# Kernel tuning notes

Measured on AMD Instinct MI355X. Metric: run time of the kernel, lower is better.

Reference implementation:

```python
import jax, jax.numpy as jnp
import numpy as np

EPS = 1e-5      # F.layer_norm default eps
ALPHA = 0.08    # ALALLaDA blend coefficient


def setup_inputs() -> dict:
    key = jax.random.key(0)
    ks = jax.random.split(key, 6)
    B, S, D, K = 2, 2048, 2048, 8
    Fh = D // 4
    h_L = jax.random.normal(ks[0], (B, S, D), jnp.float32)
    # nonzero -> masked position (stands in for input_ids == 126336)
    mask = jax.random.randint(ks[1], (B, S), 0, 2).astype(jnp.int32)
    Wr = jax.random.normal(ks[2], (K, D), jnp.float32) / np.sqrt(D).astype(np.float32)
    br = jnp.zeros((K,), jnp.float32)
    W1 = jax.random.normal(ks[3], (K, D, Fh), jnp.float32) / np.sqrt(D).astype(np.float32)
    b1 = jnp.zeros((K, Fh), jnp.float32)
    W2 = jax.random.normal(ks[4], (K, Fh, D), jnp.float32) / np.sqrt(Fh).astype(np.float32)
    b2 = jnp.zeros((K, D), jnp.float32)
    return {"h_L": h_L, "mask": mask, "Wr": Wr, "br": br,
            "W1": W1, "b1": b1, "W2": W2, "b2": b2, "range_r": 8}


def _router_blend(h_L, Wr, br, W1, b1, W2, b2, mask, range_r):
    B, S, D = h_L.shape
    masked = mask != 0
    um = (~masked).astype(h_L.dtype)  # unmasked validity [B,S]
    # Per-token, per-expert outputs M[b,s,k,d]: Linear -> exact GELU -> Linear.
    pre = jnp.einsum('bsd,kdf->bskf', h_L, W1) + b1
    M = jnp.einsum('bskf,kfd->bskd', jax.nn.gelu(pre, approximate=False), W2) + b2
    # Routing weights at every position (softmax over K experts).
    w = jax.nn.softmax(jnp.einsum('bsd,kd->bsk', h_L, Wr) + br, axis=-1)
    # Accumulate weighted expert outputs over the +/-range_r neighbor window,
    # counting only unmasked neighbors. Fixed small loop over 2r offsets.
    num = jnp.zeros((B, S, D), h_L.dtype)
    cnt = jnp.zeros((B, S), h_L.dtype)
    for o in range(-range_r, range_r + 1):
        if o == 0:
            continue
        if o > 0:  # neighbor t = a + o: shift left, zero-pad tail
            Mo = jnp.pad(M[:, o:], ((0, 0), (0, o), (0, 0), (0, 0)))
            vo = jnp.pad(um[:, o:], ((0, 0), (0, o)))
        else:      # neighbor t = a + o (o<0): shift right, zero-pad head
            Mo = jnp.pad(M[:, :o], ((0, 0), (-o, 0), (0, 0), (0, 0)))
            vo = jnp.pad(um[:, :o], ((0, 0), (-o, 0)))
        num = num + vo[..., None] * jnp.einsum('bsk,bskd->bsd', w, Mo)
        cnt = cnt + vo
    has = cnt > 0
    mean = num / jnp.maximum(cnt, 1.0)[..., None]   # mean over valid neighbors
    # layer_norm over d_model, no affine
    mu = mean.mean(-1, keepdims=True)
    var = jnp.mean((mean - mu) ** 2, axis=-1, keepdims=True)
    ln = (mean - mu) / jnp.sqrt(var + EPS)
    # delta is written only at masked positions that had >=1 neighbor
    delta = jnp.where((masked & has)[..., None], ln, 0.0)
    return h_L + ALPHA * delta


def reference(h_L, mask, Wr, br, W1, b1, W2, b2, range_r):
    return _router_blend(h_L, Wr, br, W1, b1, W2, b2, mask, range_r)
```

## Files before the change

kernel.cpp:

```cpp
#include <hip/hip_runtime.h>
#include <hip/hip_bf16.h>
#include <math.h>


#define ALPHA 0.08f
#define EPS 1e-5f

typedef __attribute__((ext_vector_type(8))) __bf16 bf16x8;
typedef __attribute__((ext_vector_type(8))) short short8;
typedef __attribute__((ext_vector_type(4))) float f32x4;

__device__ __forceinline__ unsigned short f2bf(float f) {
  unsigned u = __float_as_uint(f);
  u += 0x7fffu + ((u >> 16) & 1u);
  return (unsigned short)(u >> 16);
}
__device__ __forceinline__ float bf2f(unsigned short b) {
  return __uint_as_float(((unsigned)b) << 16);
}

#define GLD16(gptr, lptr)                                                     \
  __builtin_amdgcn_global_load_lds(                                           \
      (const __attribute__((address_space(1))) void*)(gptr),                  \
      (__attribute__((address_space(3))) void*)(lptr), 16, 0, 0)

#define LD8(p) __builtin_bit_cast(bf16x8, *(const short8*)(p))

__device__ __forceinline__ int wave_incl_scan(int v, int lane) {
#pragma unroll
  for (int off = 1; off < 64; off <<= 1) {
    int t = __shfl_up(v, off);
    if (lane >= off) v += t;
  }
  return v;
}

__global__ __launch_bounds__(256) void prep_kernel(
    const float* __restrict__ h, const int* __restrict__ mask,
    const float* __restrict__ Wr, const float* __restrict__ br,
    const float* __restrict__ W1, const float* __restrict__ W2,
    const int* __restrict__ rptr, float* __restrict__ w,
    unsigned short* __restrict__ hbc, unsigned short* __restrict__ B1t,
    unsigned short* __restrict__ B2t, int* __restrict__ ru,
    int* __restrict__ msk_idx, int* __restrict__ pos2row,
    int* __restrict__ counts) {
  const int bid = blockIdx.x;
  const int tid = threadIdx.x;
  const int lane = tid & 63, wv = tid >> 6;

  if (bid < 16384) {
    __shared__ float tile[32][33];
    int id = bid;
    const float* src;
    unsigned short* dst;
    int C, c0, r0;
    size_t dstStride;
    if (id < 8192) {
      const int k = id >> 10, rem = id & 1023;
      src = W1 + (size_t)k * 2048 * 512;
      dst = B1t + (size_t)k * 512 * 2048;
      C = 512; dstStride = 2048;
      c0 = (rem >> 6) * 32; r0 = (rem & 63) * 32;
    } else {
      id -= 8192;
      const int k = id >> 10, rem = id & 1023;
      src = W2 + (size_t)k * 512 * 2048;
      dst = B2t + (size_t)k * 512;
      C = 2048; dstStride = 4096;
      c0 = (rem >> 4) * 32; r0 = (rem & 15) * 32;
    }
    const int tx = tid & 31, ty = tid >> 5;
#pragma unroll
    for (int i = 0; i < 4; ++i)
      tile[ty + 8 * i][tx] = src[(size_t)(r0 + ty + 8 * i) * C + (c0 + tx)];
    __syncthreads();
#pragma unroll
    for (int i = 0; i < 4; ++i) {
      const int c = c0 + ty + 8 * i;
      dst[(size_t)c * dstStride + (size_t)(r0 + tx)] =
          f2bf(tile[tx][ty + 8 * i]);
    }
    return;
  }

  if (bid < 20480) {
    const int a = bid - 16384;
    const size_t base = (size_t)a * 2048;
    const int d0 = tid * 8;
    float hv[8];
    *(float4*)(hv) = *(const float4*)(h + base + d0);
    *(float4*)(hv + 4) = *(const float4*)(h + base + d0 + 4);
    float acc[8];
#pragma unroll
    for (int k = 0; k < 8; ++k) {
      float wvv[8];
      *(float4*)(wvv) = *(const float4*)(Wr + (size_t)k * 2048 + d0);
      *(float4*)(wvv + 4) = *(const float4*)(Wr + (size_t)k * 2048 + d0 + 4);
      float s = 0.f;
#pragma unroll
      for (int j = 0; j < 8; ++j) s += hv[j] * wvv[j];
      acc[k] = s;
    }
    int c0n = 0;
    {
      const int4* m4p = (const int4*)mask;
#pragma unroll
      for (int q = 0; q < 4; ++q) {
        const int4 v = m4p[tid * 4 + q];
        const int b0 = tid * 16 + q * 4;
        c0n += (v.x == 0 && b0 + 0 < a);
        c0n += (v.y == 0 && b0 + 1 < a);
        c0n += (v.z == 0 && b0 + 2 < a);
        c0n += (v.w == 0 && b0 + 3 < a);
      }
    }
#pragma unroll
    for (int off = 32; off > 0; off >>= 1) {
      c0n += __shfl_down(c0n, off);
#pragma unroll
      for (int k = 0; k < 8; ++k) acc[k] += __shfl_down(acc[k], off);
    }
    __shared__ float red[4][8];
    __shared__ float logits[8];
    __shared__ int rucnt[4];
    __shared__ int rubc;
    if (lane == 0) {
#pragma unroll
      for (int k = 0; k < 8; ++k) red[wv][k] = acc[k];
      rucnt[wv] = c0n;
    }
    __syncthreads();
    if (tid < 8)
      logits[tid] =
          red[0][tid] + red[1][tid] + red[2][tid] + red[3][tid] + br[tid];
    if (tid == 0) rubc = rucnt[0] + rucnt[1] + rucnt[2] + rucnt[3];
    __syncthreads();
    if (tid == 0) {
      float mx = logits[0];
#pragma unroll
      for (int k = 1; k < 8; ++k) mx = fmaxf(mx, logits[k]);
      float e[8], se = 0.f;
#pragma unroll
      for (int k = 0; k < 8; ++k) {
        e[k] = expf(logits[k] - mx);
        se += e[k];
      }
      const float is = 1.f / se;
#pragma unroll
      for (int k = 0; k < 8; ++k) w[(size_t)a * 8 + k] = e[k] * is;
    }
    if (mask[a] == 0) {
      const int i = rubc;
      short8 o;
#pragma unroll
      for (int j = 0; j < 8; ++j) o[j] = (short)f2bf(hv[j]);
      *(short8*)(hbc + (size_t)i * 2048 + d0) = o;
    }
    return;
  }

  {
    __shared__ int sru[4097];
    __shared__ int wsum[4];
    __shared__ int wsum2[4];
    const int t0 = tid * 16;
    int mv[16];
    {
      const int4* p = (const int4*)mask;
#pragma unroll
      for (int q = 0; q < 4; ++q) {
        const int4 v = p[tid * 4 + q];
        mv[q * 4 + 0] = v.x; mv[q * 4 + 1] = v.y;
        mv[q * 4 + 2] = v.z; mv[q * 4 + 3] = v.w;
      }
    }
    int f[16];
    int c = 0;
#pragma unroll
    for (int e = 0; e < 16; ++e) { f[e] = (mv[e] == 0); c += f[e]; }
    const int isc = wave_incl_scan(c, lane);
    if (lane == 63) wsum[wv] = isc;
    __syncthreads();
    if (tid == 0) {
      int accs = 0;
#pragma unroll
      for (int i = 0; i < 4; ++i) { int v = wsum[i]; wsum[i] = accs; accs += v; }
      sru[4096] = accs;
      ru[4096] = accs;
      counts[0] = accs;
    }
    __syncthreads();
    int ex = wsum[wv] + isc - c;
#pragma unroll
    for (int e = 0; e < 16; ++e) {
      sru[t0 + e] = ex;
      ru[t0 + e] = ex;
      ex += f[e];
    }
    __syncthreads();
    const int r = rptr[0];
    int g[16];
    int c2 = 0;
#pragma unroll
    for (int e = 0; e < 16; ++e) {
      const int t = t0 + e;
      const int s = t & 2047, tb = t & ~2047;
      const int lo = max(s - r, 0), hi = min(s + r, 2047);
      const int cnt = sru[tb + hi + 1] - sru[tb + lo];
      g[e] = (mv[e] != 0 && cnt > 0) ? 1 : 0;
      c2 += g[e];
    }
    const int isc2 = wave_incl_scan(c2, lane);
    if (lane == 63) wsum2[wv] = isc2;
    __syncthreads();
    if (tid == 0) {
      int accs = 0;
#pragma unroll
      for (int i = 0; i < 4; ++i) { int v = wsum2[i]; wsum2[i] = accs; accs += v; }
      counts[1] = accs;
    }
    __syncthreads();
    int ex2 = wsum2[wv] + isc2 - c2;
#pragma unroll
    for (int e = 0; e < 16; ++e) {
      const int t = t0 + e;
      pos2row[t] = g[e] ? ex2 : -1;
      if (g[e]) msk_idx[ex2] = t;
      ex2 += g[e];
    }
  }
}

template <int EPI>
__global__ __launch_bounds__(256, 4) void gemm_bt_kernel(
    const unsigned short* __restrict__ A, const unsigned short* __restrict__ Bt,
    float* __restrict__ Cf0, float* __restrict__ Cf1,
    unsigned short* __restrict__ Cb, const float* __restrict__ bias,
    const int* __restrict__ counts, int cidx, int N, int Kstride, int Kd) {
  const int Mlim = counts[cidx];
  const int bm = blockIdx.y * 64;
  if (bm >= Mlim) return;
  const int bn = blockIdx.x * 128;
  const int kofs = blockIdx.z * Kd;
  constexpr int SBUF = 6144;
  __shared__ __align__(16) unsigned short L[3 * SBUF];
  const int tid = threadIdx.x;
  const int lane = tid & 63;
  const int wid = tid >> 6;
  const int wr = wid >> 1;
  const int wc = wid & 1;

  f32x4 acc[2][4];
#pragma unroll
  for (int m = 0; m < 2; ++m)
#pragma unroll
    for (int n = 0; n < 4; ++n) acc[m][n] = (f32x4){0.f, 0.f, 0.f, 0.f};

  const int l4 = lane >> 2;
  const int scol = (lane & 3) * 8;
  const unsigned short* gA0 =
      A + (size_t)(bm + wid * 16 + l4) * Kstride + kofs + scol;
  const unsigned short* gB0 =
      Bt + (size_t)(bn + wid * 32 + l4) * Kstride + kofs + scol;
  const unsigned short* gB1 = gB0 + (size_t)16 * Kstride;

  const int koff = (lane >> 4) * 8;
  const int aoff = (wr * 32 + (lane & 15)) * 32 + koff;
  const int boff = 2048 + (wc * 64 + (lane & 15)) * 32 + koff;

#define STAGE(buf, t)                                                         \
  {                                                                           \
    const int k0_ = (t) << 5;                                                 \
    unsigned short* la_ = L + (buf) * SBUF + wid * 512;                       \
    unsigned short* lb_ = L + (buf) * SBUF + 2048 + wid * 1024;               \
    GLD16(gA0 + k0_, la_);                                                    \
    GLD16(gB0 + k0_, lb_);                                                    \
    GLD16(gB1 + k0_, lb_ + 512);                                              \
  }

#define COMPUTE(buf)                                                          \
  {                                                                           \
    const unsigned short* bb_ = L + (buf) * SBUF;                             \
    bf16x8 af[2], bfr[4];                                                     \
    _Pragma("unroll") for (int m = 0; m < 2; ++m) af[m] =                     \
        LD8(bb_ + aoff + m * 512);                                            \
    _Pragma("unroll") for (int n = 0; n < 4; ++n) bfr[n] =                    \
        LD8(bb_ + boff + n * 512);                                            \
    _Pragma("unroll") for (int m = 0; m < 2; ++m)                             \
        _Pragma("unroll") for (int n = 0; n < 4; ++n) acc[m][n] =             \
            __builtin_amdgcn_mfma_f32_16x16x32_bf16(af[m], bfr[n],            \
                                                    acc[m][n], 0, 0, 0);      \
  }

  const int nt = Kd >> 5;
  STAGE(0, 0);
  STAGE(1, 1);
  int cb = 0, sb = 2;
#pragma unroll 1
  for (int t = 0; t < nt - 2; ++t) {
    asm volatile("s_waitcnt vmcnt(3)" ::: "memory");
    __builtin_amdgcn_s_barrier();
    __builtin_amdgcn_sched_barrier(0);
    STAGE(sb, t + 2);
    COMPUTE(cb);
    cb = (cb == 2) ? 0 : cb + 1;
    sb = (sb == 2) ? 0 : sb + 1;
  }
  asm volatile("s_waitcnt vmcnt(3)" ::: "memory");
  __builtin_amdgcn_s_barrier();
  __builtin_amdgcn_sched_barrier(0);
  COMPUTE(cb);
  cb = (cb == 2) ? 0 : cb + 1;
  asm volatile("s_waitcnt vmcnt(0)" ::: "memory");
  __builtin_amdgcn_s_barrier();
  __builtin_amdgcn_sched_barrier(0);
  COMPUTE(cb);
#undef STAGE
#undef COMPUTE

  float* __restrict__ Cf = (blockIdx.z == 0) ? Cf0 : Cf1;
  const int r0 = bm + wr * 32 + (lane >> 4) * 4;
  const int c0 = bn + wc * 64 + (lane & 15);
#pragma unroll
  for (int m = 0; m < 2; ++m) {
#pragma unroll
    for (int n = 0; n < 4; ++n) {
      const int col = c0 + n * 16;
#pragma unroll
      for (int ii = 0; ii < 4; ++ii) {
        const int row = r0 + m * 16 + ii;
        if (row >= Mlim) continue;
        const size_t off = (size_t)row * N + col;
        float v = acc[m][n][ii];
        if (EPI == 1) {
          v += bias[col];
          v = 0.5f * v * (1.0f + erff(v * 0.70710678118654752f));
          Cb[off] = f2bf(v);
        } else {
          Cf[off] = v;
        }
      }
    }
  }
}

__global__ __launch_bounds__(256) void window_kernel(
    const unsigned short* __restrict__ Act_c, const float* __restrict__ w,
    const int* __restrict__ ru, const int* __restrict__ pos2row,
    const int* __restrict__ rptr, unsigned short* __restrict__ G_c) {
  const int tid = threadIdx.x;
  const int b = blockIdx.y >> 7;
  const int seg = blockIdx.y & 127;
  const int s0 = seg * 16;
  const int tb = b * 2048;
  const int cbase = blockIdx.x * 2048 + tid * 8;
  const int kx = cbase >> 9;
  const int r = rptr[0];

  float W[8] = {0.f, 0.f, 0.f, 0.f, 0.f, 0.f, 0.f, 0.f};
  for (int t = s0 - r; t <= s0 + r; ++t) {
    if (t < 0 || t > 2047) continue;
    const int j = ru[tb + t];
    if (ru[tb + t + 1] > j) {
      const short8 v = *(const short8*)(Act_c + (size_t)j * 4096 + cbase);
#pragma unroll
      for (int e = 0; e < 8; ++e) W[e] += bf2f((unsigned short)v[e]);
    }
  }
#pragma unroll 1
  for (int i = 0; i < 16; ++i) {
    const int t = s0 + i;
    const int a = tb + t;
    const int rowo = pos2row[a];
    if (rowo >= 0) {
      const float wv = w[(size_t)a * 8 + kx];
      short8 o8;
#pragma unroll
      for (int e = 0; e < 8; ++e) o8[e] = (short)f2bf(W[e] * wv);
      *(short8*)(G_c + (size_t)rowo * 4096 + cbase) = o8;
    }
    const int tin = t + r + 1;
    if (tin < 2048) {
      const int j = ru[tb + tin];
      if (ru[tb + tin + 1] > j) {
        const short8 v = *(const short8*)(Act_c + (size_t)j * 4096 + cbase);
#pragma unroll
        for (int e = 0; e < 8; ++e) W[e] += bf2f((unsigned short)v[e]);
      }
    }
    const int tout = t - r;
    if (tout >= 0) {
      const int j = ru[tb + tout];
      if (ru[tb + tout + 1] > j) {
        const short8 v = *(const short8*)(Act_c + (size_t)j * 4096 + cbase);
#pragma unroll
        for (int e = 0; e < 8; ++e) W[e] -= bf2f((unsigned short)v[e]);
      }
    }
  }
}

__global__ void final_kernel(const float* __restrict__ h,
                             const int* __restrict__ pos2row,
                             const float* __restrict__ w,
                             const float* __restrict__ b2,
                             const float* __restrict__ p0,
                             const float* __restrict__ p1,
                             const int* __restrict__ ru,
                             const int* __restrict__ rptr,
                             float* __restrict__ out) {
  const int a = blockIdx.x;
  const int tid = threadIdx.x;
  const int lane = tid & 63, wid = tid >> 6;
  const size_t base = (size_t)a * 2048;
  const int d0 = tid * 8;
  const int row = pos2row[a];
  if (row < 0) {
    const float4 x0 = *(const float4*)(h + base + d0);
    const float4 x1 = *(const float4*)(h + base + d0 + 4);
    *(float4*)(out + base + d0) = x0;
    *(float4*)(out + base + d0 + 4) = x1;
    return;
  }
  const int s = a & 2047;
  const int tb = a & ~2047;
  const int r = rptr[0];
  const int lo = max(s - r, 0), hi = min(s + r, 2047);
  const int cnt = ru[tb + hi + 1] - ru[tb + lo];
  float wk[8];
#pragma unroll
  for (int k = 0; k < 8; ++k) wk[k] = w[(size_t)a * 8 + k];
  const float cntf = (float)cnt;
  const float icnt = 1.0f / cntf;
  float mval[8];
  float s1 = 0.f, s2 = 0.f;
#pragma unroll
  for (int j = 0; j < 8; ++j) {
    const int d = d0 + j;
    float wb2 = 0.f;
#pragma unroll
    for (int k = 0; k < 8; ++k) wb2 += wk[k] * b2[(size_t)k * 2048 + d];
    const size_t po = (size_t)row * 2048 + d;
    const float v = (p0[po] + p1[po] + cntf * wb2) * icnt;
    mval[j] = v;
    s1 += v;
    s2 += v * v;
  }
#pragma unroll
  for (int off = 32; off > 0; off >>= 1) {
    s1 += __shfl_down(s1, off);
    s2 += __shfl_down(s2, off);
  }
  __shared__ float red[8];
  if (lane == 0) {
    red[wid] = s1;
    red[4 + wid] = s2;
  }
  __syncthreads();
  const float S1 = red[0] + red[1] + red[2] + red[3];
  const float S2 = red[4] + red[5] + red[6] + red[7];
  const float mu = S1 * (1.0f / 2048.0f);
  const float var = S2 * (1.0f / 2048.0f) - mu * mu;
  const float rin = rsqrtf(var + EPS);
#pragma unroll
  for (int j = 0; j < 8; ++j) {
    const int d = d0 + j;
    out[base + d] = h[base + d] + ALPHA * ((mval[j] - mu) * rin);
  }
}

extern "C" void kernel_launch(void* const* d_in, const int* in_sizes, int n_in,
                              void* d_out, int out_size, void* d_ws,
                              size_t ws_size, hipStream_t stream) {
  const float* h = (const float*)d_in[0];
  const int* mask = (const int*)d_in[1];
  const float* Wr = (const float*)d_in[2];
  const float* br = (const float*)d_in[3];
  const float* W1 = (const float*)d_in[4];
  const float* b1 = (const float*)d_in[5];
  const float* W2 = (const float*)d_in[6];
  const float* b2 = (const float*)d_in[7];
  const int* rptr = (const int*)d_in[8];
  float* out = (float*)d_out;

  char* ws = (char*)d_ws;
  unsigned short* hbc = (unsigned short*)(ws + 0);
  unsigned short* B1t = (unsigned short*)(ws + 16777216);
  unsigned short* B2t = (unsigned short*)(ws + 33554432);
  unsigned short* Act_c = (unsigned short*)(ws + 50331648);
  unsigned short* G_c = (unsigned short*)(ws + 83886080);
  float* p0 = (float*)(ws + 50331648);
  float* p1 = (float*)(ws + 0);
  float* wbuf = (float*)(ws + 117440512);
  int* ru = (int*)(ws + 117571584);
  int* msk_idx = ru + 4100;
  int* pos2row = msk_idx + 4096;
  int* counts = pos2row + 4096;

  prep_kernel<<<20481, 256, 0, stream>>>(h, mask, Wr, br, W1, W2, rptr, wbuf,
                                         hbc, B1t, B2t, ru, msk_idx, pos2row,
                                         counts);
  gemm_bt_kernel<1><<<dim3(32, 64, 1), 256, 0, stream>>>(
      hbc, B1t, nullptr, nullptr, Act_c, b1, counts, 0, 4096, 2048, 2048);
  window_kernel<<<dim3(2, 256), 256, 0, stream>>>(Act_c, wbuf, ru, pos2row,
                                                  rptr, G_c);
  gemm_bt_kernel<0><<<dim3(16, 64, 2), 256, 0, stream>>>(
      G_c, B2t, p0, p1, nullptr, nullptr, counts, 1, 2048, 4096, 2048);
  final_kernel<<<4096, 256, 0, stream>>>(h, pos2row, wbuf, b2, p0, p1, ru,
                                         rptr, out);
}
```

Baseline: 338.5 us.

## Enlarge GEMM tiles to 128x256 with 8 waves and phased ping-pong schedule

```diff
diff --git a/kernel.cpp b/kernel.cpp
--- a/kernel.cpp
+++ b/kernel.cpp
@@ -232,97 +232,149 @@
 }
 
 template <int EPI>
-__global__ __launch_bounds__(256, 4) void gemm_bt_kernel(
+__global__ __launch_bounds__(512, 2) void gemm8p_kernel(
     const unsigned short* __restrict__ A, const unsigned short* __restrict__ Bt,
     float* __restrict__ Cf0, float* __restrict__ Cf1,
     unsigned short* __restrict__ Cb, const float* __restrict__ bias,
     const int* __restrict__ counts, int cidx, int N, int Kstride, int Kd) {
   const int Mlim = counts[cidx];
-  const int bm = blockIdx.y * 64;
+  const int bm = blockIdx.y * 128;
   if (bm >= Mlim) return;
-  const int bn = blockIdx.x * 128;
+  const int bn = blockIdx.x * 256;
   const int kofs = blockIdx.z * Kd;
-  constexpr int SBUF = 6144;
+  constexpr int SA = 8192;
+  constexpr int SBUF = 24576;
   __shared__ __align__(16) unsigned short L[3 * SBUF];
   const int tid = threadIdx.x;
   const int lane = tid & 63;
   const int wid = tid >> 6;
-  const int wr = wid >> 1;
-  const int wc = wid & 1;
-
-  f32x4 acc[2][4];
-#pragma unroll
-  for (int m = 0; m < 2; ++m)
+  const int wr = wid >> 2;
+  const int wc = wid & 3;
+
+  f32x4 acc[4][4];
+#pragma unroll
+  for (int m = 0; m < 4; ++m)
 #pragma unroll
     for (int n = 0; n < 4; ++n) acc[m][n] = (f32x4){0.f, 0.f, 0.f, 0.f};
 
-  const int l4 = lane >> 2;
-  const int scol = (lane & 3) * 8;
-  const unsigned short* gA0 =
-      A + (size_t)(bm + wid * 16 + l4) * Kstride + kofs + scol;
-  const unsigned short* gB0 =
-      Bt + (size_t)(bn + wid * 32 + l4) * Kstride + kofs + scol;
-  const unsigned short* gB1 = gB0 + (size_t)16 * Kstride;
-
-  const int koff = (lane >> 4) * 8;
-  const int aoff = (wr * 32 + (lane & 15)) * 32 + koff;
-  const int boff = 2048 + (wc * 64 + (lane & 15)) * 32 + koff;
-
-#define STAGE(buf, t)                                                         \
+  const int trow = tid >> 3;
+  const int scol = ((tid & 7) ^ (trow & 7)) * 8;
+  const unsigned short* gA =
+      A + (size_t)(bm + trow) * Kstride + kofs + scol;
+  const unsigned short* gB =
+      Bt + (size_t)(bn + trow) * Kstride + kofs + scol;
+  unsigned short* const ld0 = (unsigned short*)L + tid * 8;
+
+  const int x7 = lane & 7;
+  const int t16 = lane >> 4;
+  const int s0 = (t16 ^ x7) * 8;
+  const int s1 = ((4 + t16) ^ x7) * 8;
+  const int arow = (wr * 64 + (lane & 15)) * 64;
+  const int brow = SA + (wc * 64 + (lane & 15)) * 64;
+
+  bf16x8 afr[2][2], b0f[2][2], b1f[2][2];
+
+#define STAGE_A(buf, k0)                                                      \
   {                                                                           \
-    const int k0_ = (t) << 5;                                                 \
-    unsigned short* la_ = L + (buf) * SBUF + wid * 512;                       \
-    unsigned short* lb_ = L + (buf) * SBUF + 2048 + wid * 1024;               \
-    GLD16(gA0 + k0_, la_);                                                    \
-    GLD16(gB0 + k0_, lb_);                                                    \
-    GLD16(gB1 + k0_, lb_ + 512);                                              \
-  }
-
-#define COMPUTE(buf)                                                          \
+    unsigned short* d_ = ld0 + (buf) * SBUF;                                  \
+    GLD16(gA + (k0), d_);                                                     \
+    GLD16(gA + (size_t)64 * Kstride + (k0), d_ + 4096);                       \
+  }
+#define STAGE_B0(buf, k0)                                                     \
   {                                                                           \
-    const unsigned short* bb_ = L + (buf) * SBUF;                             \
-    bf16x8 af[2], bfr[4];                                                     \
-    _Pragma("unroll") for (int m = 0; m < 2; ++m) af[m] =                     \
-        LD8(bb_ + aoff + m * 512);                                            \
-    _Pragma("unroll") for (int n = 0; n < 4; ++n) bfr[n] =                    \
-        LD8(bb_ + boff + n * 512);                                            \
-    _Pragma("unroll") for (int m = 0; m < 2; ++m)                             \
-        _Pragma("unroll") for (int n = 0; n < 4; ++n) acc[m][n] =             \
-            __builtin_amdgcn_mfma_f32_16x16x32_bf16(af[m], bfr[n],            \
-                                                    acc[m][n], 0, 0, 0);      \
-  }
-
-  const int nt = Kd >> 5;
-  STAGE(0, 0);
-  STAGE(1, 1);
-  int cb = 0, sb = 2;
+    unsigned short* d_ = ld0 + (buf) * SBUF + SA;                             \
+    GLD16(gB + (k0), d_);                                                     \
+    GLD16(gB + (size_t)64 * Kstride + (k0), d_ + 4096);                       \
+  }
+#define STAGE_B1(buf, k0)                                                     \
+  {                                                                           \
+    unsigned short* d_ = ld0 + (buf) * SBUF + SA + 8192;                      \
+    GLD16(gB + (size_t)128 * Kstride + (k0), d_);                             \
+    GLD16(gB + (size_t)192 * Kstride + (k0), d_ + 4096);                      \
+  }
+#define RD_A(cb_, half)                                                       \
+  _Pragma("unroll") for (int m = 0; m < 2; ++m) {                             \
+    afr[m][0] = LD8((cb_) + arow + ((half) * 2 + m) * 1024 + s0);             \
+    afr[m][1] = LD8((cb_) + arow + ((half) * 2 + m) * 1024 + s1);             \
+  }
+#define RD_B(cb_, half, bf)                                                   \
+  _Pragma("unroll") for (int n = 0; n < 2; ++n) {                             \
+    bf[n][0] = LD8((cb_) + brow + ((half) * 2 + n) * 1024 + s0);              \
+    bf[n][1] = LD8((cb_) + brow + ((half) * 2 + n) * 1024 + s1);              \
+  }
+#define QMFMA(mb, nb, bf)                                                     \
+  _Pragma("unroll") for (int m = 0; m < 2; ++m)                               \
+      _Pragma("unroll") for (int n = 0; n < 2; ++n) {                         \
+    acc[(mb) + m][(nb) + n] = __builtin_amdgcn_mfma_f32_16x16x32_bf16(        \
+        afr[m][0], bf[n][0], acc[(mb) + m][(nb) + n], 0, 0, 0);               \
+    acc[(mb) + m][(nb) + n] = __builtin_amdgcn_mfma_f32_16x16x32_bf16(        \
+        afr[m][1], bf[n][1], acc[(mb) + m][(nb) + n], 0, 0, 0);               \
+  }
+#define PHASE_SYNC                                                            \
+  __builtin_amdgcn_s_barrier();                                               \
+  asm volatile("s_waitcnt lgkmcnt(0)" ::: "memory");                          \
+  __builtin_amdgcn_sched_barrier(0);
+
+  const int nt = Kd >> 6;
+  STAGE_A(0, 0); STAGE_B0(0, 0); STAGE_B1(0, 0);
+  STAGE_A(1, 64); STAGE_B0(1, 64); STAGE_B1(1, 64);
+  asm volatile("s_waitcnt vmcnt(6)" ::: "memory");
+  __builtin_amdgcn_s_barrier();
+
 #pragma unroll 1
-  for (int t = 0; t < nt - 2; ++t) {
-    asm volatile("s_waitcnt vmcnt(3)" ::: "memory");
+  for (int t = 0; t < nt; ++t) {
+    const int cbuf = t % 3;
+    const int sbuf = (t + 2) % 3;
+    const unsigned short* cb_ = (const unsigned short*)L + cbuf * SBUF;
+    const bool st = (t + 2) < nt;
+    const int k2 = (t + 2) << 6;
+    RD_A(cb_, 0);
+    RD_B(cb_, 0, b0f);
+    if (st) STAGE_A(sbuf, k2);
+    PHASE_SYNC;
+    __builtin_amdgcn_s_setprio(1);
+    QMFMA(0, 0, b0f);
+    __builtin_amdgcn_s_setprio(0);
+    __builtin_amdgcn_s_barrier();
+    RD_B(cb_, 1, b1f);
+    if (st) STAGE_B0(sbuf, k2);
+    PHASE_SYNC;
+    __builtin_amdgcn_s_setprio(1);
+    QMFMA(0, 2, b1f);
+    __builtin_amdgcn_s_setprio(0);
+    __builtin_amdgcn_s_barrier();
+    RD_A(cb_, 1);
+    if (st) STAGE_B1(sbuf, k2);
+    PHASE_SYNC;
+    __builtin_amdgcn_s_setprio(1);
+    QMFMA(2, 2, b1f);
+    __builtin_amdgcn_s_setprio(0);
+    __builtin_amdgcn_s_barrier();
+    if (t < nt - 2) {
+      asm volatile("s_waitcnt vmcnt(6)" ::: "memory");
+    } else {
+      asm volatile("s_waitcnt vmcnt(0)" ::: "memory");
+    }
     __builtin_amdgcn_s_barrier();
     __builtin_amdgcn_sched_barrier(0);
-    STAGE(sb, t + 2);
-    COMPUTE(cb);
-    cb = (cb == 2) ? 0 : cb + 1;
-    sb = (sb == 2) ? 0 : sb + 1;
-  }
-  asm volatile("s_waitcnt vmcnt(3)" ::: "memory");
-  __builtin_amdgcn_s_barrier();
-  __builtin_amdgcn_sched_barrier(0);
-  COMPUTE(cb);
-  cb = (cb == 2) ? 0 : cb + 1;
-  asm volatile("s_waitcnt vmcnt(0)" ::: "memory");
-  __builtin_amdgcn_s_barrier();
-  __builtin_amdgcn_sched_barrier(0);
-  COMPUTE(cb);
-#undef STAGE
-#undef COMPUTE
+    __builtin_amdgcn_s_setprio(1);
+    QMFMA(2, 0, b0f);
+    __builtin_amdgcn_s_setprio(0);
+    __builtin_amdgcn_s_barrier();
+  }
+#undef STAGE_A
+#undef STAGE_B0
+#undef STAGE_B1
+#undef RD_A
+#undef RD_B
+#undef QMFMA
+#undef PHASE_SYNC
 
   float* __restrict__ Cf = (blockIdx.z == 0) ? Cf0 : Cf1;
-  const int r0 = bm + wr * 32 + (lane >> 4) * 4;
+  const int r0 = bm + wr * 64 + (lane >> 4) * 4;
   const int c0 = bn + wc * 64 + (lane & 15);
 #pragma unroll
-  for (int m = 0; m < 2; ++m) {
+  for (int m = 0; m < 4; ++m) {
 #pragma unroll
     for (int n = 0; n < 4; ++n) {
       const int col = c0 + n * 16;
@@ -500,11 +552,11 @@
   prep_kernel<<<20481, 256, 0, stream>>>(h, mask, Wr, br, W1, W2, rptr, wbuf,
                                          hbc, B1t, B2t, ru, msk_idx, pos2row,
                                          counts);
-  gemm_bt_kernel<1><<<dim3(32, 64, 1), 256, 0, stream>>>(
+  gemm8p_kernel<1><<<dim3(16, 32, 1), 512, 0, stream>>>(
       hbc, B1t, nullptr, nullptr, Act_c, b1, counts, 0, 4096, 2048, 2048);
   window_kernel<<<dim3(2, 256), 256, 0, stream>>>(Act_c, wbuf, ru, pos2row,
                                                   rptr, G_c);
-  gemm_bt_kernel<0><<<dim3(16, 64, 2), 256, 0, stream>>>(
+  gemm8p_kernel<0><<<dim3(8, 32, 2), 512, 0, stream>>>(
       G_c, B2t, p0, p1, nullptr, nullptr, counts, 1, 2048, 4096, 2048);
   final_kernel<<<4096, 256, 0, stream>>>(h, pos2row, wbuf, b2, p0, p1, ru,
                                          rptr, out);
```

Result: no change. 332.5 us (-1.8%).
